# Kernel optimization log

Hardware: AMD Instinct MI355X
Metric: run time of the kernel (lower is better)

## Reference

```python
import jax, jax.numpy as jnp
import numpy as np

BBOX_POS_MAX = 1024.0
BN_EPS = 1e-5


def _bn_eval(x, g, b, rm, rv):
    # BatchNorm1d in eval mode: affine transform with running stats
    return g * (x - rm) * jax.lax.rsqrt(rv + BN_EPS) + b


def setup_inputs() -> dict:
    key = jax.random.key(0)
    ks = jax.random.split(key, 24)
    B, N, F = 32, 512, 1024
    E = 32768
    H1, H2, H3 = 512, 256, 128          # node_pred_hidden
    EH1, EH2 = 64, 64                   # edge_pred_hidden
    NC, EC = 8, 10                      # node/edge concept channels
    BC = 9                              # bbox_channels (4 bbox + 4 dir + 1 prio)
    s = 0.02
    inp = {
        'roi_features': jax.random.normal(ks[0], (B, N, F), jnp.float32),
        'batch_bboxes': jax.random.uniform(ks[1], (B, N, 4), jnp.float32) * BBOX_POS_MAX,
        'batch_directions': jax.random.uniform(ks[2], (B, N, 4), jnp.float32),
        'batch_priorities': jax.random.uniform(ks[3], (B, N), jnp.float32),
        'batch_edge_index': jax.random.randint(ks[4], (B, 2, E), 0, N, jnp.int32),
        # node_predictor params
        'np_w1': jax.random.normal(ks[5], (F, H1), jnp.float32) * s,
        'np_b1': jnp.zeros((H1,), jnp.float32),
        'bn1_g': jnp.ones((H1,), jnp.float32),
        'bn1_b': jnp.zeros((H1,), jnp.float32),
        'bn1_rm': jnp.zeros((H1,), jnp.float32),
        'bn1_rv': jnp.ones((H1,), jnp.float32),
        'np_w2': jax.random.normal(ks[6], (H1, H2), jnp.float32) * s,
        'np_b2': jnp.zeros((H2,), jnp.float32),
        'bn2_g': jnp.ones((H2,), jnp.float32),
        'bn2_b': jnp.zeros((H2,), jnp.float32),
        'bn2_rm': jnp.zeros((H2,), jnp.float32),
        'bn2_rv': jnp.ones((H2,), jnp.float32),
        'np_w3': jax.random.normal(ks[7], (H2, H3), jnp.float32) * s,
        'np_b3': jnp.zeros((H3,), jnp.float32),
        'ni_w': jax.random.normal(ks[8], (H3, NC), jnp.float32) * s,
        'ni_b': jnp.zeros((NC,), jnp.float32),
        # edge_predictor params (input dim = 2 * bbox_channels)
        'ep_w1': jax.random.normal(ks[9], (2 * BC, EH1), jnp.float32) * s,
        'ep_b1': jnp.zeros((EH1,), jnp.float32),
        'ep_w2': jax.random.normal(ks[10], (EH1, EH2), jnp.float32) * s,
        'ep_b2': jnp.zeros((EH2,), jnp.float32),
        'ei_w': jax.random.normal(ks[11], (EH2, EC), jnp.float32) * s,
        'ei_b': jnp.zeros((EC,), jnp.float32),
    }
    return inp


def reference(roi_features, batch_bboxes, batch_directions, batch_priorities,
              batch_edge_index,
              np_w1, np_b1, bn1_g, bn1_b, bn1_rm, bn1_rv,
              np_w2, np_b2, bn2_g, bn2_b, bn2_rm, bn2_rv,
              np_w3, np_b3, ni_w, ni_b,
              ep_w1, ep_b1, ep_w2, ep_b2, ei_w, ei_b):
    B, N, F = roi_features.shape
    # ---- node path: MLP (eval-mode BN, dropout = identity) + sigmoid interpreter
    x = roi_features.reshape(B * N, F)
    h = jax.nn.relu(_bn_eval(x @ np_w1 + np_b1, bn1_g, bn1_b, bn1_rm, bn1_rv))
    h = jax.nn.relu(_bn_eval(h @ np_w2 + np_b2, bn2_g, bn2_b, bn2_rm, bn2_rv))
    h = jax.nn.relu(h @ np_w3 + np_b3)
    node_concepts = jax.nn.sigmoid(h @ ni_w + ni_b).reshape(B, N, -1)
    # ---- edge path: per-batch gather of node attrs via edge_index, concat, MLP
    node_attr = jnp.concatenate(
        [batch_bboxes / BBOX_POS_MAX, batch_directions, batch_priorities[..., None]],
        axis=-1)  # [B, N, 9]
    C = node_attr.shape[-1]
    src_idx = batch_edge_index[:, 0, :, None]  # [B, E, 1]
    dst_idx = batch_edge_index[:, 1, :, None]
    src = jnp.take_along_axis(node_attr, src_idx.astype(jnp.int32), axis=1)  # [B, E, 9]
    dst = jnp.take_along_axis(node_attr, dst_idx.astype(jnp.int32), axis=1)
    edge_attr = jnp.concatenate([src, dst], axis=-1).reshape(-1, 2 * C)  # [B*E, 18]
    e = jax.nn.relu(edge_attr @ ep_w1 + ep_b1)
    e = jax.nn.relu(e @ ep_w2 + ep_b2)
    edge_concepts = jax.nn.sigmoid(e @ ei_w + ei_b)  # [B*E, EC]
    return node_concepts, edge_concepts
```

## Files before the change

### kernel.cpp

```cpp
#include <hip/hip_runtime.h>
#include <cstdint>
#include <cstddef>

#define BN_EPSF 1e-5f

constexpr int B_  = 32, N_ = 512, F_ = 1024, E_ = 32768;
constexpr int H1_ = 512, H2_ = 256, H3_ = 128, NC_ = 8, EC_ = 10;
constexpr int M_  = B_ * N_;
constexpr int NE_ = B_ * E_;

typedef short bf16x8 __attribute__((ext_vector_type(8)));
typedef float f32x4  __attribute__((ext_vector_type(4)));

__device__ __forceinline__ short f2bf(float f) {
  union { float f; unsigned u; } v; v.f = f;
  unsigned r = v.u + 0x7fffu + ((v.u >> 16) & 1u);
  return (short)(r >> 16);
}
__device__ __forceinline__ unsigned rnepack(float a, float b) {
  unsigned ua = __float_as_uint(a); ua = ua + 0x7fffu + ((ua >> 16) & 1u);
  unsigned ub = __float_as_uint(b); ub = ub + 0x7fffu + ((ub >> 16) & 1u);
  return __builtin_amdgcn_perm(ub, ua, 0x07060302u);
}

#define GLDS(gp, lp) __builtin_amdgcn_global_load_lds( \
    (const __attribute__((address_space(1))) void*)(gp), \
    (__attribute__((address_space(3))) void*)(lp), 16, 0, 0)

#define MFMA(a, b, c) __builtin_amdgcn_mfma_f32_16x16x32_bf16((a), (b), (c), 0, 0, 0)

__device__ __forceinline__ void wt_body(
    const float* __restrict__ W, short* __restrict__ Wt, int K, int N,
    int bx, int by, float (*s)[33])
{
  const int tx = threadIdx.x & 31, ty = threadIdx.x >> 5;
  const int k0 = by * 32, n0 = bx * 32;
#pragma unroll
  for (int r = 0; r < 4; r++)
    s[ty * 4 + r][tx] = W[(size_t)(k0 + ty * 4 + r) * N + n0 + tx];
  __syncthreads();
#pragma unroll
  for (int r = 0; r < 4; r++)
    Wt[(size_t)(n0 + ty * 4 + r) * K + k0 + tx] = f2bf(s[tx][ty * 4 + r]);
}

__global__ __launch_bounds__(256) void k_prep(
    const float* __restrict__ roi, ushort* __restrict__ roiB,
    const float* __restrict__ w1, short* __restrict__ w1t,
    const float* __restrict__ w2, short* __restrict__ w2t,
    const float* __restrict__ w3, short* __restrict__ w3t)
{
  __shared__ float s[32][33];
  const int bx = blockIdx.x;
  if (bx < 8192) {
    int i = bx * 256 + threadIdx.x;
    float4 a = *(const float4*)(roi + (size_t)i * 8);
    float4 b = *(const float4*)(roi + (size_t)i * 8 + 4);
    unsigned o[4];
    o[0] = rnepack(a.x, a.y); o[1] = rnepack(a.z, a.w);
    o[2] = rnepack(b.x, b.y); o[3] = rnepack(b.z, b.w);
    *(uint4*)(roiB + (size_t)i * 8) = *(uint4*)o;
  } else if (bx < 8704) {
    int idx = bx - 8192; wt_body(w1, w1t, F_, H1_, idx & 15, idx >> 4, s);
  } else if (bx < 8832) {
    int idx = bx - 8704; wt_body(w2, w2t, H1_, H2_, idx & 7, idx >> 3, s);
  } else {
    int idx = bx - 8832; wt_body(w3, w3t, H2_, H3_, idx & 3, idx >> 2, s);
  }
}

__global__ __launch_bounds__(256, 3) void k_fused(
    const float* __restrict__ bbox, const float* __restrict__ dir,
    const float* __restrict__ pri, const int* __restrict__ eidx,
    const float* __restrict__ ew1, const float* __restrict__ eb1,
    const float* __restrict__ ew2, const float* __restrict__ eb2,
    const float* __restrict__ eow, const float* __restrict__ eob,
    float* __restrict__ out_edge,
    const short* __restrict__ roiB, const short* __restrict__ w1t,
    const float* __restrict__ b1, const float* __restrict__ g1,
    const float* __restrict__ bb1, const float* __restrict__ rm1,
    const float* __restrict__ rv1, short* __restrict__ h1)
{
  __shared__ __align__(16) char arena[49728];

  const int bx = blockIdx.x;
  const int rsel = bx % 3;
  const int tid  = threadIdx.x;
  const int wave = tid >> 6, lane = tid & 63;
  const int lm = lane & 15;

  if (rsel == 2) {
    const int lb = bx / 3;
    short* As = (short*)arena;
    short* Bs = (short*)(arena + 8192);
    const int m0 = (lb >> 2) * 128, n0 = (lb & 3) * 128;
    const int wm = wave >> 1, wn = wave & 1;
    const int arow = tid >> 2;
    const int akq  = (tid & 3) * 8;

    f32x4 acc[4][4] = {};
    for (int k0 = 0; k0 < F_; k0 += 32) {
#pragma unroll
      for (int it = 0; it < 2; it++)
        GLDS(roiB + (size_t)(m0 + it * 64 + arow) * F_ + k0 + akq,
             (char*)As + it * 4096 + wave * 1024);
#pragma unroll
      for (int it = 0; it < 2; it++)
        GLDS(w1t + (size_t)(n0 + it * 64 + arow) * F_ + k0 + akq,
             (char*)Bs + it * 4096 + wave * 1024);
      __syncthreads();

      const int ko = (lane >> 4) * 8;
      bf16x8 af[4], bfr[4];
#pragma unroll
      for (int t = 0; t < 4; t++) {
        af[t]  = *(const bf16x8*)&As[(wm * 64 + t * 16 + lm) * 32 + ko];
        bfr[t] = *(const bf16x8*)&Bs[(wn * 64 + t * 16 + lm) * 32 + ko];
      }
#pragma unroll
      for (int ti = 0; ti < 4; ti++)
#pragma unroll
        for (int tj = 0; tj < 4; tj++)
          acc[ti][tj] = MFMA(af[ti], bfr[tj], acc[ti][tj]);
      __syncthreads();
    }
#pragma unroll
    for (int tj = 0; tj < 4; tj++) {
      const int col = n0 + wn * 64 + tj * 16 + lm;
      const float bi = b1[col];
      float s = g1[col] * rsqrtf(rv1[col] + BN_EPSF);
      float t = bb1[col] - rm1[col] * s;
#pragma unroll
      for (int ti = 0; ti < 4; ti++) {
        const int rbase = m0 + wm * 64 + ti * 16 + ((lane >> 4) << 2);
#pragma unroll
        for (int r = 0; r < 4; r++) {
          float v = fmaf(acc[ti][tj][r] + bi, s, t);
          h1[(size_t)(rbase + r) * H1_ + col] = f2bf(fmaxf(v, 0.f));
        }
      }
    }
    return;
  }

  const int eb = (bx / 3) * 2 + rsel;
  const int batch = eb >> 5;
  const int e_base = eb * 1024;

  short* sA    = (short*)arena;
  short* sH1   = (short*)(arena + 18432);
  ushort* sAttr= (ushort*)(arena + 36864);
  float* sB    = (float*)(arena + 49152);

  short* sW1 = sA;
  short* sW2 = sA + 2048;
  short* sW3 = sA + 6144;
  short* sX  = sA;
  short* sH2 = sA;

  const int lk8 = (lane >> 4) * 8;
  const int lr  = (lane >> 4) * 4;

  for (int i = tid; i < 2048; i += 256) {
    int n = i >> 5, k = i & 31;
    sW1[i] = (k < 18) ? f2bf(ew1[k * 64 + n]) : (short)0;
  }
  for (int i = tid; i < 4096; i += 256) {
    int n = i >> 6, k = i & 63;
    sW2[i] = f2bf(ew2[k * 64 + n]);
  }
  for (int i = tid; i < 1024; i += 256) {
    int n = i >> 6, k = i & 63;
    sW3[i] = (n < 10) ? f2bf(eow[k * 10 + n]) : (short)0;
  }
  if (tid < 64) { sB[tid] = eb1[tid]; sB[64 + tid] = eb2[tid]; }
  if (tid < 16) sB[128 + tid] = (tid < 10) ? eob[tid] : 0.f;
  {
    const float inv = 1.0f / 1024.0f;
    for (int n = tid; n < 512; n += 256) {
      int gi = batch * 512 + n;
      float4 bv = *(const float4*)(bbox + (size_t)gi * 4);
      float4 dv = *(const float4*)(dir + (size_t)gi * 4);
      float pp = pri[gi];
      unsigned* row = (unsigned*)&sAttr[n * 12];
      uint2 a, c, e;
      a.x = rnepack(bv.x * inv, bv.y * inv); a.y = rnepack(bv.z * inv, bv.w * inv);
      c.x = rnepack(dv.x, dv.y);             c.y = rnepack(dv.z, dv.w);
      e.x = rnepack(pp, 0.f);                e.y = 0;
      *(uint2*)(row + 0) = a; *(uint2*)(row + 2) = c; *(uint2*)(row + 4) = e;
    }
  }
  __syncthreads();

  bf16x8 fW1[4], fW2[4][2], fW3[2];
#pragma unroll
  for (int t = 0; t < 4; t++)
    fW1[t] = *(const bf16x8*)&sW1[(t * 16 + lm) * 32 + lk8];
#pragma unroll
  for (int t = 0; t < 4; t++)
#pragma unroll
    for (int ks = 0; ks < 2; ks++)
      fW2[t][ks] = *(const bf16x8*)&sW2[(t * 16 + lm) * 64 + ks * 32 + lk8];
#pragma unroll
  for (int ks = 0; ks < 2; ks++)
    fW3[ks] = *(const bf16x8*)&sW3[lm * 64 + ks * 32 + lk8];
  float bias1v[4], bias2v[4];
#pragma unroll
  for (int t = 0; t < 4; t++) {
    bias1v[t] = sB[t * 16 + lm];
    bias2v[t] = sB[64 + t * 16 + lm];
  }
  const float biasOv = sB[128 + lm];
  __syncthreads();

  const int* ei = eidx + (size_t)batch * 2 * E_;

  for (int bi = 0; bi < 8; bi++) {
    const int e0 = e_base + bi * 128;

    if (tid < 128) {
      int kk = (e0 + tid) & (E_ - 1);
      int s = ei[kk], d = ei[E_ + kk];
      const unsigned* ps = (const unsigned*)&sAttr[s * 12];
      const unsigned* pd = (const unsigned*)&sAttr[d * 12];
      uint2 s01 = *(const uint2*)(ps);
      uint2 s23 = *(const uint2*)(ps + 2);
      uint2 s45 = *(const uint2*)(ps + 4);
      uint2 d01 = *(const uint2*)(pd);
      uint2 d23 = *(const uint2*)(pd + 2);
      uint2 d45 = *(const uint2*)(pd + 4);
      unsigned x[16];
      x[0] = s01.x; x[1] = s01.y; x[2] = s23.x; x[3] = s23.y;
      x[4] = (s45.x & 0xffffu) | (d01.x << 16);
      x[5] = (d01.x >> 16) | (d01.y << 16);
      x[6] = (d01.y >> 16) | (d23.x << 16);
      x[7] = (d23.x >> 16) | (d23.y << 16);
      x[8] = (d23.y >> 16) | (d45.x << 16);
#pragma unroll
      for (int i = 9; i < 16; i++) x[i] = 0;
      unsigned* row = (unsigned*)&sX[tid * 40];
      *(uint4*)(row + 0)  = *(uint4*)&x[0];
      *(uint4*)(row + 4)  = *(uint4*)&x[4];
      *(uint4*)(row + 8)  = *(uint4*)&x[8];
      *(uint4*)(row + 12) = *(uint4*)&x[12];
    }
    __syncthreads();

    bf16x8 a1f[2];
#pragma unroll
    for (int ti = 0; ti < 2; ti++)
      a1f[ti] = *(const bf16x8*)&sX[(wave * 32 + ti * 16 + lm) * 40 + lk8];
    f32x4 acc1[2][4] = {};
#pragma unroll
    for (int ti = 0; ti < 2; ti++)
#pragma unroll
      for (int tj = 0; tj < 4; tj++)
        acc1[ti][tj] = MFMA(a1f[ti], fW1[tj], acc1[ti][tj]);
#pragma unroll
    for (int ti = 0; ti < 2; ti++)
#pragma unroll
      for (int tj = 0; tj < 4; tj++)
#pragma unroll
        for (int r = 0; r < 4; r++) {
          int row = wave * 32 + ti * 16 + lr + r;
          float v = acc1[ti][tj][r] + bias1v[tj];
          sH1[row * 72 + tj * 16 + lm] = f2bf(fmaxf(v, 0.f));
        }
    __syncthreads();

    bf16x8 a2f[2][2];
#pragma unroll
    for (int ti = 0; ti < 2; ti++)
#pragma unroll
      for (int ks = 0; ks < 2; ks++)
        a2f[ti][ks] = *(const bf16x8*)&sH1[(wave * 32 + ti * 16 + lm) * 72 + ks * 32 + lk8];
    f32x4 acc2[2][4] = {};
#pragma unroll
    for (int ks = 0; ks < 2; ks++)
#pragma unroll
      for (int ti = 0; ti < 2; ti++)
#pragma unroll
        for (int tj = 0; tj < 4; tj++)
          acc2[ti][tj] = MFMA(a2f[ti][ks], fW2[tj][ks], acc2[ti][tj]);
#pragma unroll
    for (int ti = 0; ti < 2; ti++)
#pragma unroll
      for (int tj = 0; tj < 4; tj++)
#pragma unroll
        for (int r = 0; r < 4; r++) {
          int row = wave * 32 + ti * 16 + lr + r;
          float v = acc2[ti][tj][r] + bias2v[tj];
          sH2[row * 72 + tj * 16 + lm] = f2bf(fmaxf(v, 0.f));
        }

    bf16x8 a3f[2][2];
#pragma unroll
    for (int ti = 0; ti < 2; ti++)
#pragma unroll
      for (int ks = 0; ks < 2; ks++)
        a3f[ti][ks] = *(const bf16x8*)&sH2[(wave * 32 + ti * 16 + lm) * 72 + ks * 32 + lk8];
    f32x4 acc3[2] = {};
#pragma unroll
    for (int ks = 0; ks < 2; ks++)
#pragma unroll
      for (int ti = 0; ti < 2; ti++)
        acc3[ti] = MFMA(a3f[ti][ks], fW3[ks], acc3[ti]);
    if (lm < 10) {
#pragma unroll
      for (int ti = 0; ti < 2; ti++)
#pragma unroll
        for (int r = 0; r < 4; r++) {
          int row = wave * 32 + ti * 16 + lr + r;
          float v = acc3[ti][r] + biasOv;
          out_edge[(size_t)(e0 + row) * 10 + lm] = 1.f / (1.f + __expf(-v));
        }
    }
    __syncthreads();
  }
}

__global__ __launch_bounds__(256) void k_tail(
    const short* __restrict__ h1, const short* __restrict__ w2t,
    const short* __restrict__ w3t,
    const float* __restrict__ b2, const float* __restrict__ g2,
    const float* __restrict__ bb2, const float* __restrict__ rm2,
    const float* __restrict__ rv2,
    const float* __restrict__ b3, const float* __restrict__ niw,
    const float* __restrict__ nib, float* __restrict__ out)
{
  __shared__ __align__(16) char arena[53760];
  short* sA  = (short*)arena;
  short* sB  = (short*)(arena + 4096);
  short* sH2 = (short*)(arena + 36864);
  short* sB3 = (short*)arena;
  short* sH3 = (short*)(arena + 16384);

  const int tid  = threadIdx.x;
  const int wave = tid >> 6, lane = tid & 63;
  const int lm = lane & 15, q = lane >> 4;
  const int wm = wave >> 1, wn = wave & 1;
  const int m0 = blockIdx.x * 32;
  const int srow = tid >> 2;
  const int skq  = (tid & 3) * 8;

  f32x4 acc2[8] = {};
  for (int k0 = 0; k0 < 512; k0 += 64) {
    {
      int c = tid >> 7, row = (tid >> 2) & 31;
      GLDS(h1 + (size_t)(m0 + row) * 512 + k0 + c * 32 + skq,
           (char*)sA + wave * 1024);
    }
#pragma unroll
    for (int it = 0; it < 4; it++)
#pragma unroll
      for (int c = 0; c < 2; c++)
        GLDS(w2t + (size_t)(it * 64 + srow) * 512 + k0 + c * 32 + skq,
             (char*)sB + c * 16384 + it * 4096 + wave * 1024);
    __syncthreads();
#pragma unroll
    for (int c = 0; c < 2; c++) {
      bf16x8 af = *(const bf16x8*)&sA[c * 1024 + (wm * 16 + lm) * 32 + q * 8];
#pragma unroll
      for (int nt = 0; nt < 8; nt++) {
        bf16x8 bfr = *(const bf16x8*)&sB[c * 8192 + (wn * 128 + nt * 16 + lm) * 32 + q * 8];
        acc2[nt] = MFMA(af, bfr, acc2[nt]);
      }
    }
    __syncthreads();
  }
#pragma unroll
  for (int nt = 0; nt < 8; nt++) {
    int col = wn * 128 + nt * 16 + lm;
    float s = g2[col] * rsqrtf(rv2[col] + BN_EPSF);
    float t = bb2[col] - rm2[col] * s;
    float bi = b2[col];
#pragma unroll
    for (int r = 0; r < 4; r++) {
      float v = fmaf(acc2[nt][r] + bi, s, t);
      sH2[(wm * 16 + q * 4 + r) * 264 + col] = f2bf(fmaxf(v, 0.f));
    }
  }
  __syncthreads();

  f32x4 acc3[4] = {};
  for (int k0 = 0; k0 < 256; k0 += 64) {
#pragma unroll
    for (int it = 0; it < 2; it++)
#pragma unroll
      for (int c = 0; c < 2; c++)
        GLDS(w3t + (size_t)(it * 64 + srow) * 256 + k0 + c * 32 + skq,
             (char*)sB3 + c * 8192 + it * 4096 + wave * 1024);
    __syncthreads();
#pragma unroll
    for (int c = 0; c < 2; c++) {
      bf16x8 af = *(const bf16x8*)&sH2[(wm * 16 + lm) * 264 + k0 + c * 32 + q * 8];
#pragma unroll
      for (int nt = 0; nt < 4; nt++) {
        bf16x8 bfr = *(const bf16x8*)&sB3[c * 4096 + (wn * 64 + nt * 16 + lm) * 32 + q * 8];
        acc3[nt] = MFMA(af, bfr, acc3[nt]);
      }
    }
    __syncthreads();
  }
#pragma unroll
  for (int nt = 0; nt < 4; nt++) {
    int col = wn * 64 + nt * 16 + lm;
    float bi = b3[col];
#pragma unroll
    for (int r = 0; r < 4; r++) {
      float v = acc3[nt][r] + bi;
      sH3[(wm * 16 + q * 4 + r) * 136 + col] = f2bf(fmaxf(v, 0.f));
    }
  }
  __syncthreads();

  if (wave < 2) {
    f32x4 a4 = {};
#pragma unroll
    for (int c = 0; c < 4; c++) {
      ushort tmp[8];
#pragma unroll
      for (int j = 0; j < 8; j++) {
        int k = c * 32 + q * 8 + j;
        tmp[j] = (lm < 8) ? (ushort)f2bf(niw[k * 8 + lm]) : (ushort)0;
      }
      bf16x8 fw = *(bf16x8*)tmp;
      bf16x8 af4 = *(const bf16x8*)&sH3[(wave * 16 + lm) * 136 + c * 32 + q * 8];
      a4 = MFMA(af4, fw, a4);
    }
    if (lm < 8) {
      float bi = nib[lm];
#pragma unroll
      for (int r = 0; r < 4; r++) {
        float v = a4[r] + bi;
        out[(size_t)(m0 + wave * 16 + q * 4 + r) * 8 + lm] = 1.f / (1.f + __expf(-v));
      }
    }
  }
}

extern "C" void kernel_launch(void* const* d_in, const int* in_sizes, int n_in,
                              void* d_out, int out_size, void* d_ws, size_t ws_size,
                              hipStream_t stream)
{
  const float* roi   = (const float*)d_in[0];
  const float* bbox  = (const float*)d_in[1];
  const float* dir   = (const float*)d_in[2];
  const float* pri   = (const float*)d_in[3];
  const int*   eidx  = (const int*)d_in[4];
  const float* w1    = (const float*)d_in[5];
  const float* b1    = (const float*)d_in[6];
  const float* g1    = (const float*)d_in[7];
  const float* bb1   = (const float*)d_in[8];
  const float* rm1   = (const float*)d_in[9];
  const float* rv1   = (const float*)d_in[10];
  const float* w2    = (const float*)d_in[11];
  const float* b2    = (const float*)d_in[12];
  const float* g2    = (const float*)d_in[13];
  const float* bb2   = (const float*)d_in[14];
  const float* rm2   = (const float*)d_in[15];
  const float* rv2   = (const float*)d_in[16];
  const float* w3    = (const float*)d_in[17];
  const float* b3    = (const float*)d_in[18];
  const float* niw   = (const float*)d_in[19];
  const float* nib   = (const float*)d_in[20];
  const float* ew1   = (const float*)d_in[21];
  const float* eb1   = (const float*)d_in[22];
  const float* ew2   = (const float*)d_in[23];
  const float* eb2   = (const float*)d_in[24];
  const float* eow   = (const float*)d_in[25];
  const float* eob   = (const float*)d_in[26];

  float* out_node = (float*)d_out;
  float* out_edge = (float*)d_out + (size_t)M_ * NC_;

  char* w = (char*)d_ws;
  short*  roiB = (short*)w;
  short*  w1t  = (short*)(w + 33554432);
  short*  w2t  = (short*)(w + 34603008);
  short*  w3t  = (short*)(w + 34865152);
  short*  h1   = (short*)(w + 35717120);

  k_prep<<<8864, 256, 0, stream>>>(roi, (ushort*)roiB, w1, w1t, w2, w2t,
                                   w3, w3t);

  k_fused<<<1536, 256, 0, stream>>>(
      bbox, dir, pri, eidx, ew1, eb1, ew2, eb2, eow, eob, out_edge,
      roiB, w1t, b1, g1, bb1, rm1, rv1, h1);

  k_tail<<<M_ / 32, 256, 0, stream>>>(
      h1, w2t, w3t, b2, g2, bb2, rm2, rv2, b3, niw, nib, out_node);
}
```

Measured before the change: 252.3 us.

## Keep edge MLP activations in registers via transposed MFMA and lane shuffles

Restructures the edge MLP in the fused kernel so weights act as the MFMA A operand and edges as B. Each layer's ReLU output is repacked to bf16 with cross-lane shuffles instead of being written to and reread from LDS. This drops the per-batch LDS staging buffers and most __syncthreads, and cuts the shared arena size, which could allow more resident blocks. It also folds biases into the accumulator init, uses the hardware v_cvt_pk_bf16_f32 instruction for float-to-bf16 conversion everywhere, and writes edge outputs as float2 vectors. The cost is more shuffle instructions and extra register pressure.

```diff
diff --git a/kernel.cpp b/kernel.cpp
--- a/kernel.cpp
+++ b/kernel.cpp
@@ -17,10 +17,10 @@
   unsigned r = v.u + 0x7fffu + ((v.u >> 16) & 1u);
   return (short)(r >> 16);
 }
-__device__ __forceinline__ unsigned rnepack(float a, float b) {
-  unsigned ua = __float_as_uint(a); ua = ua + 0x7fffu + ((ua >> 16) & 1u);
-  unsigned ub = __float_as_uint(b); ub = ub + 0x7fffu + ((ub >> 16) & 1u);
-  return __builtin_amdgcn_perm(ub, ua, 0x07060302u);
+__device__ __forceinline__ unsigned cvtpk(float a, float b) {
+  unsigned r;
+  asm("v_cvt_pk_bf16_f32 %0, %1, %2" : "=v"(r) : "v"(a), "v"(b));
+  return r;
 }
 
 #define GLDS(gp, lp) __builtin_amdgcn_global_load_lds( \
@@ -57,8 +57,8 @@
     float4 a = *(const float4*)(roi + (size_t)i * 8);
     float4 b = *(const float4*)(roi + (size_t)i * 8 + 4);
     unsigned o[4];
-    o[0] = rnepack(a.x, a.y); o[1] = rnepack(a.z, a.w);
-    o[2] = rnepack(b.x, b.y); o[3] = rnepack(b.z, b.w);
+    o[0] = cvtpk(a.x, a.y); o[1] = cvtpk(a.z, a.w);
+    o[2] = cvtpk(b.x, b.y); o[3] = cvtpk(b.z, b.w);
     *(uint4*)(roiB + (size_t)i * 8) = *(uint4*)o;
   } else if (bx < 8704) {
     int idx = bx - 8192; wt_body(w1, w1t, F_, H1_, idx & 15, idx >> 4, s);
@@ -66,6 +66,34 @@
     int idx = bx - 8704; wt_body(w2, w2t, H1_, H2_, idx & 7, idx >> 3, s);
   } else {
     int idx = bx - 8832; wt_body(w3, w3t, H2_, H3_, idx & 3, idx >> 2, s);
+  }
+}
+
+__device__ __forceinline__ void relu_pack_shuf(
+    const f32x4 (&acc)[4], int la, int lb, bool lo32, bf16x8 (&out)[2])
+{
+  unsigned plo[4], phi[4];
+#pragma unroll
+  for (int t = 0; t < 4; t++) {
+    plo[t] = cvtpk(fmaxf(acc[t][0], 0.f), fmaxf(acc[t][1], 0.f));
+    phi[t] = cvtpk(fmaxf(acc[t][2], 0.f), fmaxf(acc[t][3], 0.f));
+  }
+#pragma unroll
+  for (int ks = 0; ks < 2; ks++) {
+    unsigned w0a = (unsigned)__shfl((int)plo[2 * ks], la);
+    unsigned w0b = (unsigned)__shfl((int)plo[2 * ks + 1], la);
+    unsigned w1a = (unsigned)__shfl((int)phi[2 * ks], la);
+    unsigned w1b = (unsigned)__shfl((int)phi[2 * ks + 1], la);
+    unsigned w2a = (unsigned)__shfl((int)plo[2 * ks], lb);
+    unsigned w2b = (unsigned)__shfl((int)plo[2 * ks + 1], lb);
+    unsigned w3a = (unsigned)__shfl((int)phi[2 * ks], lb);
+    unsigned w3b = (unsigned)__shfl((int)phi[2 * ks + 1], lb);
+    union { unsigned u[4]; bf16x8 v; } t;
+    t.u[0] = lo32 ? w0a : w0b;
+    t.u[1] = lo32 ? w1a : w1b;
+    t.u[2] = lo32 ? w2a : w2b;
+    t.u[3] = lo32 ? w3a : w3b;
+    out[ks] = t.v;
   }
 }
 
@@ -81,7 +109,7 @@
     const float* __restrict__ bb1, const float* __restrict__ rm1,
     const float* __restrict__ rv1, short* __restrict__ h1)
 {
-  __shared__ __align__(16) char arena[49728];
+  __shared__ __align__(16) char arena[30720];
 
   const int bx = blockIdx.x;
   const int rsel = bx % 3;
@@ -134,36 +162,33 @@
       for (int ti = 0; ti < 4; ti++) {
         const int rbase = m0 + wm * 64 + ti * 16 + ((lane >> 4) << 2);
 #pragma unroll
-        for (int r = 0; r < 4; r++) {
-          float v = fmaf(acc[ti][tj][r] + bi, s, t);
-          h1[(size_t)(rbase + r) * H1_ + col] = f2bf(fmaxf(v, 0.f));
+        for (int r = 0; r < 4; r += 2) {
+          float va = fmaf(acc[ti][tj][r]     + bi, s, t);
+          float vb = fmaf(acc[ti][tj][r + 1] + bi, s, t);
+          unsigned p = cvtpk(fmaxf(va, 0.f), fmaxf(vb, 0.f));
+          h1[(size_t)(rbase + r)     * H1_ + col] = (short)p;
+          h1[(size_t)(rbase + r + 1) * H1_ + col] = (short)(p >> 16);
         }
       }
     }
     return;
   }
 
-  const int eb = (bx / 3) * 2 + rsel;
+  const int eb    = (bx / 3) * 2 + rsel;
   const int batch = eb >> 5;
-  const int e_base = eb * 1024;
-
-  short* sA    = (short*)arena;
-  short* sH1   = (short*)(arena + 18432);
-  ushort* sAttr= (ushort*)(arena + 36864);
-  float* sB    = (float*)(arena + 49152);
-
-  short* sW1 = sA;
-  short* sW2 = sA + 2048;
-  short* sW3 = sA + 6144;
-  short* sX  = sA;
-  short* sH2 = sA;
-
-  const int lk8 = (lane >> 4) * 8;
-  const int lr  = (lane >> 4) * 4;
+  const int q     = lane >> 4;
+
+  short*  sW1   = (short*)arena;
+  short*  sW2   = (short*)(arena + 4096);
+  short*  sW3   = (short*)(arena + 12288);
+  ushort* sAttr = (ushort*)(arena + 14336);
 
   for (int i = tid; i < 2048; i += 256) {
     int n = i >> 5, k = i & 31;
-    sW1[i] = (k < 18) ? f2bf(ew1[k * 64 + n]) : (short)0;
+    short v = 0;
+    if (k < 9)                  v = f2bf(ew1[k * 64 + n]);
+    else if (k >= 16 && k < 25) v = f2bf(ew1[(k - 7) * 64 + n]);
+    sW1[i] = v;
   }
   for (int i = tid; i < 4096; i += 256) {
     int n = i >> 6, k = i & 63;
@@ -173,8 +198,6 @@
     int n = i >> 6, k = i & 63;
     sW3[i] = (n < 10) ? f2bf(eow[k * 10 + n]) : (short)0;
   }
-  if (tid < 64) { sB[tid] = eb1[tid]; sB[64 + tid] = eb2[tid]; }
-  if (tid < 16) sB[128 + tid] = (tid < 10) ? eob[tid] : 0.f;
   {
     const float inv = 1.0f / 1024.0f;
     for (int n = tid; n < 512; n += 256) {
@@ -182,140 +205,102 @@
       float4 bv = *(const float4*)(bbox + (size_t)gi * 4);
       float4 dv = *(const float4*)(dir + (size_t)gi * 4);
       float pp = pri[gi];
-      unsigned* row = (unsigned*)&sAttr[n * 12];
-      uint2 a, c, e;
-      a.x = rnepack(bv.x * inv, bv.y * inv); a.y = rnepack(bv.z * inv, bv.w * inv);
-      c.x = rnepack(dv.x, dv.y);             c.y = rnepack(dv.z, dv.w);
-      e.x = rnepack(pp, 0.f);                e.y = 0;
-      *(uint2*)(row + 0) = a; *(uint2*)(row + 2) = c; *(uint2*)(row + 4) = e;
+      uint4 lo, hi;
+      lo.x = cvtpk(bv.x * inv, bv.y * inv); lo.y = cvtpk(bv.z * inv, bv.w * inv);
+      lo.z = cvtpk(dv.x, dv.y);             lo.w = cvtpk(dv.z, dv.w);
+      hi.x = cvtpk(pp, 0.f); hi.y = 0; hi.z = 0; hi.w = 0;
+      *(uint4*)&sAttr[n * 16]     = lo;
+      *(uint4*)&sAttr[n * 16 + 8] = hi;
     }
   }
   __syncthreads();
 
-  bf16x8 fW1[4], fW2[4][2], fW3[2];
-#pragma unroll
-  for (int t = 0; t < 4; t++)
-    fW1[t] = *(const bf16x8*)&sW1[(t * 16 + lm) * 32 + lk8];
-#pragma unroll
-  for (int t = 0; t < 4; t++)
+  f32x4 b1q[4], b2q[4], boq;
+#pragma unroll
+  for (int t = 0; t < 4; t++) {
+    b1q[t] = *(const f32x4*)(eb1 + t * 16 + q * 4);
+    b2q[t] = *(const f32x4*)(eb2 + t * 16 + q * 4);
+  }
+#pragma unroll
+  for (int r = 0; r < 4; r++)
+    boq[r] = (q * 4 + r < 10) ? eob[q * 4 + r] : 0.f;
+
+  const int  la   = (lane & 15) | ((lane & 16) << 1);
+  const int  lbn  = la + 16;
+  const bool lo32 = (lane < 32);
+  const int* ip   = eidx + (size_t)batch * 2 * E_ + ((lane >= 32) ? E_ : 0);
+  const int  ebl  = (eb & 31) * 1024;
+  const int  ah   = (lane & 16) ? 16 : 0;
+
+  for (int bi = 0; bi < 8; bi++) {
+    const int kb = ebl + bi * 128 + wave * 32 + lm;
+
+    bf16x8 xf[2];
+#pragma unroll
+    for (int ti = 0; ti < 2; ti++) {
+      int kk   = (kb + ti * 16) & (E_ - 1);
+      int node = ip[kk];
+      xf[ti] = *(const bf16x8*)&sAttr[node * 16 + ah];
+    }
+
+    f32x4 acc1[2][4];
+#pragma unroll
+    for (int tj = 0; tj < 4; tj++) {
+      bf16x8 fw1 = *(const bf16x8*)&sW1[(tj * 16 + lm) * 32 + q * 8];
+#pragma unroll
+      for (int ti = 0; ti < 2; ti++)
+        acc1[ti][tj] = MFMA(fw1, xf[ti], b1q[tj]);
+    }
+    bf16x8 xf2[2][2];
+#pragma unroll
+    for (int ti = 0; ti < 2; ti++)
+      relu_pack_shuf(acc1[ti], la, lbn, lo32, xf2[ti]);
+
+    f32x4 acc2[2][4];
+#pragma unroll
+    for (int ti = 0; ti < 2; ti++)
+#pragma unroll
+      for (int tj = 0; tj < 4; tj++)
+        acc2[ti][tj] = b2q[tj];
 #pragma unroll
     for (int ks = 0; ks < 2; ks++)
-      fW2[t][ks] = *(const bf16x8*)&sW2[(t * 16 + lm) * 64 + ks * 32 + lk8];
-#pragma unroll
-  for (int ks = 0; ks < 2; ks++)
-    fW3[ks] = *(const bf16x8*)&sW3[lm * 64 + ks * 32 + lk8];
-  float bias1v[4], bias2v[4];
-#pragma unroll
-  for (int t = 0; t < 4; t++) {
-    bias1v[t] = sB[t * 16 + lm];
-    bias2v[t] = sB[64 + t * 16 + lm];
-  }
-  const float biasOv = sB[128 + lm];
-  __syncthreads();
-
-  const int* ei = eidx + (size_t)batch * 2 * E_;
-
-  for (int bi = 0; bi < 8; bi++) {
-    const int e0 = e_base + bi * 128;
-
-    if (tid < 128) {
-      int kk = (e0 + tid) & (E_ - 1);
-      int s = ei[kk], d = ei[E_ + kk];
-      const unsigned* ps = (const unsigned*)&sAttr[s * 12];
-      const unsigned* pd = (const unsigned*)&sAttr[d * 12];
-      uint2 s01 = *(const uint2*)(ps);
-      uint2 s23 = *(const uint2*)(ps + 2);
-      uint2 s45 = *(const uint2*)(ps + 4);
-      uint2 d01 = *(const uint2*)(pd);
-      uint2 d23 = *(const uint2*)(pd + 2);
-      uint2 d45 = *(const uint2*)(pd + 4);
-      unsigned x[16];
-      x[0] = s01.x; x[1] = s01.y; x[2] = s23.x; x[3] = s23.y;
-      x[4] = (s45.x & 0xffffu) | (d01.x << 16);
-      x[5] = (d01.x >> 16) | (d01.y << 16);
-      x[6] = (d01.y >> 16) | (d23.x << 16);
-      x[7] = (d23.x >> 16) | (d23.y << 16);
-      x[8] = (d23.y >> 16) | (d45.x << 16);
-#pragma unroll
-      for (int i = 9; i < 16; i++) x[i] = 0;
-      unsigned* row = (unsigned*)&sX[tid * 40];
-      *(uint4*)(row + 0)  = *(uint4*)&x[0];
-      *(uint4*)(row + 4)  = *(uint4*)&x[4];
-      *(uint4*)(row + 8)  = *(uint4*)&x[8];
-      *(uint4*)(row + 12) = *(uint4*)&x[12];
-    }
-    __syncthreads();
-
-    bf16x8 a1f[2];
+#pragma unroll
+      for (int tj = 0; tj < 4; tj++) {
+        bf16x8 fw2 = *(const bf16x8*)&sW2[(tj * 16 + lm) * 64 + ks * 32 + q * 8];
+#pragma unroll
+        for (int ti = 0; ti < 2; ti++)
+          acc2[ti][tj] = MFMA(fw2, xf2[ti][ks], acc2[ti][tj]);
+      }
+    bf16x8 xf3[2][2];
 #pragma unroll
     for (int ti = 0; ti < 2; ti++)
-      a1f[ti] = *(const bf16x8*)&sX[(wave * 32 + ti * 16 + lm) * 40 + lk8];
-    f32x4 acc1[2][4] = {};
-#pragma unroll
-    for (int ti = 0; ti < 2; ti++)
-#pragma unroll
-      for (int tj = 0; tj < 4; tj++)
-        acc1[ti][tj] = MFMA(a1f[ti], fW1[tj], acc1[ti][tj]);
-#pragma unroll
-    for (int ti = 0; ti < 2; ti++)
-#pragma unroll
-      for (int tj = 0; tj < 4; tj++)
-#pragma unroll
-        for (int r = 0; r < 4; r++) {
-          int row = wave * 32 + ti * 16 + lr + r;
-          float v = acc1[ti][tj][r] + bias1v[tj];
-          sH1[row * 72 + tj * 16 + lm] = f2bf(fmaxf(v, 0.f));
-        }
-    __syncthreads();
-
-    bf16x8 a2f[2][2];
-#pragma unroll
-    for (int ti = 0; ti < 2; ti++)
+      relu_pack_shuf(acc2[ti], la, lbn, lo32, xf3[ti]);
+
+    bf16x8 fw3[2];
+#pragma unroll
+    for (int ks = 0; ks < 2; ks++)
+      fw3[ks] = *(const bf16x8*)&sW3[lm * 64 + ks * 32 + q * 8];
+#pragma unroll
+    for (int ti = 0; ti < 2; ti++) {
+      f32x4 a3 = boq;
 #pragma unroll
       for (int ks = 0; ks < 2; ks++)
-        a2f[ti][ks] = *(const bf16x8*)&sH1[(wave * 32 + ti * 16 + lm) * 72 + ks * 32 + lk8];
-    f32x4 acc2[2][4] = {};
-#pragma unroll
-    for (int ks = 0; ks < 2; ks++)
-#pragma unroll
-      for (int ti = 0; ti < 2; ti++)
-#pragma unroll
-        for (int tj = 0; tj < 4; tj++)
-          acc2[ti][tj] = MFMA(a2f[ti][ks], fW2[tj][ks], acc2[ti][tj]);
-#pragma unroll
-    for (int ti = 0; ti < 2; ti++)
-#pragma unroll
-      for (int tj = 0; tj < 4; tj++)
-#pragma unroll
-        for (int r = 0; r < 4; r++) {
-          int row = wave * 32 + ti * 16 + lr + r;
-          float v = acc2[ti][tj][r] + bias2v[tj];
-          sH2[row * 72 + tj * 16 + lm] = f2bf(fmaxf(v, 0.f));
-        }
-
-    bf16x8 a3f[2][2];
-#pragma unroll
-    for (int ti = 0; ti < 2; ti++)
-#pragma unroll
-      for (int ks = 0; ks < 2; ks++)
-        a3f[ti][ks] = *(const bf16x8*)&sH2[(wave * 32 + ti * 16 + lm) * 72 + ks * 32 + lk8];
-    f32x4 acc3[2] = {};
-#pragma unroll
-    for (int ks = 0; ks < 2; ks++)
-#pragma unroll
-      for (int ti = 0; ti < 2; ti++)
-        acc3[ti] = MFMA(a3f[ti][ks], fW3[ks], acc3[ti]);
-    if (lm < 10) {
-#pragma unroll
-      for (int ti = 0; ti < 2; ti++)
-#pragma unroll
-        for (int r = 0; r < 4; r++) {
-          int row = wave * 32 + ti * 16 + lr + r;
-          float v = acc3[ti][r] + biasOv;
-          out_edge[(size_t)(e0 + row) * 10 + lm] = 1.f / (1.f + __expf(-v));
-        }
-    }
-    __syncthreads();
+        a3 = MFMA(fw3[ks], xf3[ti][ks], a3);
+      float o[4];
+#pragma unroll
+      for (int r = 0; r < 4; r++)
+        o[r] = 1.f / (1.f + __expf(-a3[r]));
+      size_t base = (size_t)(eb * 1024 + bi * 128 + wave * 32 + ti * 16 + lm) * 10;
+      if (q == 0) {
+        float2 t0; t0.x = o[0]; t0.y = o[1]; *(float2*)(out_edge + base)     = t0;
+        float2 t1; t1.x = o[2]; t1.y = o[3]; *(float2*)(out_edge + base + 2) = t1;
+      } else if (q == 1) {
+        float2 t0; t0.x = o[0]; t0.y = o[1]; *(float2*)(out_edge + base + 4) = t0;
+        float2 t1; t1.x = o[2]; t1.y = o[3]; *(float2*)(out_edge + base + 6) = t1;
+      } else if (q == 2) {
+        float2 t0; t0.x = o[0]; t0.y = o[1]; *(float2*)(out_edge + base + 8) = t0;
+      }
+    }
   }
 }
 
@@ -374,11 +359,17 @@
     float s = g2[col] * rsqrtf(rv2[col] + BN_EPSF);
     float t = bb2[col] - rm2[col] * s;
     float bi = b2[col];
-#pragma unroll
-    for (int r = 0; r < 4; r++) {
-      float v = fmaf(acc2[nt][r] + bi, s, t);
-      sH2[(wm * 16 + q * 4 + r) * 264 + col] = f2bf(fmaxf(v, 0.f));
-    }
+    float v0 = fmaf(acc2[nt][0] + bi, s, t);
+    float v1 = fmaf(acc2[nt][1] + bi, s, t);
+    float v2 = fmaf(acc2[nt][2] + bi, s, t);
+    float v3 = fmaf(acc2[nt][3] + bi, s, t);
+    unsigned p01 = cvtpk(fmaxf(v0, 0.f), fmaxf(v1, 0.f));
+    unsigned p23 = cvtpk(fmaxf(v2, 0.f), fmaxf(v3, 0.f));
+    int rb = wm * 16 + q * 4;
+    sH2[(rb + 0) * 264 + col] = (short)p01;
+    sH2[(rb + 1) * 264 + col] = (short)(p01 >> 16);
+    sH2[(rb + 2) * 264 + col] = (short)p23;
+    sH2[(rb + 3) * 264 + col] = (short)(p23 >> 16);
   }
   __syncthreads();
 
@@ -406,11 +397,17 @@
   for (int nt = 0; nt < 4; nt++) {
     int col = wn * 64 + nt * 16 + lm;
     float bi = b3[col];
-#pragma unroll
-    for (int r = 0; r < 4; r++) {
-      float v = acc3[nt][r] + bi;
-      sH3[(wm * 16 + q * 4 + r) * 136 + col] = f2bf(fmaxf(v, 0.f));
-    }
+    float v0 = acc3[nt][0] + bi;
+    float v1 = acc3[nt][1] + bi;
+    float v2 = acc3[nt][2] + bi;
+    float v3 = acc3[nt][3] + bi;
+    unsigned p01 = cvtpk(fmaxf(v0, 0.f), fmaxf(v1, 0.f));
+    unsigned p23 = cvtpk(fmaxf(v2, 0.f), fmaxf(v3, 0.f));
+    int rb = wm * 16 + q * 4;
+    sH3[(rb + 0) * 136 + col] = (short)p01;
+    sH3[(rb + 1) * 136 + col] = (short)(p01 >> 16);
+    sH3[(rb + 2) * 136 + col] = (short)p23;
+    sH3[(rb + 3) * 136 + col] = (short)(p23 >> 16);
   }
   __syncthreads();
 
```

Measured after the change: 255.1 us. Within noise of the previous version (+1.1%).
